# Optimization experiments

Hardware: AMD Instinct MI355X
Metric: run time of the kernel (lower is better)

The kernel has to match this reference:

```python
import jax, jax.numpy as jnp
import numpy as np


def setup_inputs() -> dict:
    key = jax.random.key(0)
    k1, k2, k3 = jax.random.split(key, 3)
    B, L, D, K = 4, 4096, 2048, 4
    x = jax.random.normal(k1, (B, L, D), dtype=jnp.float32)
    # depthwise kernel, channel-last layout (K, 1, D); torch weight is (D,1,K) = w.transpose(2,1,0)
    w = jax.random.normal(k2, (K, 1, D), dtype=jnp.float32) * 0.1
    b = jax.random.normal(k3, (D,), dtype=jnp.float32) * 0.1
    return {"x": x, "w": w, "b": b}


def reference(x, w, b):
    """Depthwise causal conv1d, channel-last.
    x: (B, L, D); w: (K, 1, D); b: (D,). Returns (B, L, D).
    Matches torch: Conv1d(D, D, K, groups=D, padding=K-1)(x.T)[..., :L].T
    which is exactly a causal conv (left pad K-1, trim to L).
    """
    K = w.shape[0]
    D = x.shape[-1]
    y = jax.lax.conv_general_dilated(
        x, w,
        window_strides=(1,),
        padding=[(K - 1, 0)],  # causal: left pad only
        feature_group_count=D,
        dimension_numbers=("NWC", "WIO", "NWC"),
    )
    return y + b
```

## Files before the change

### kernel.cpp

```cpp
#include <hip/hip_runtime.h>
#include <stdint.h>


#define CB 4
#define CL 4096
#define CD 2048
#define STRIP 256
#define HALO 3
#define WROWS 32
#define NSTRIP (CD / STRIP)
#define NSEG (CL / (WROWS * 4))

typedef float nfloat4 __attribute__((ext_vector_type(4)));

__global__ __launch_bounds__(256, 4) void short_conv_kernel(
    const float* __restrict__ x,
    const float* __restrict__ w,
    const float* __restrict__ bias,
    float* __restrict__ y)
{
    const int tid  = threadIdx.x;
    const int lane = tid & 63;
    const int wv   = tid >> 6;

    const int bid   = blockIdx.x;
    const int strip = bid & (NSTRIP - 1);
    const int seg   = (bid >> 3) & (NSEG - 1);
    const int b     = bid >> 8;

    const int r0 = (seg * 4 + wv) * WROWS;
    const int c0 = strip * STRIP;

    const float* xs = x + (size_t)b * CL * CD + c0 + lane * 4;
    float*       ys = y + (size_t)b * CL * CD + c0 + lane * 4;

    const float4 w0 = *(const float4*)(w + 0 * CD + c0 + lane * 4);
    const float4 w1 = *(const float4*)(w + 1 * CD + c0 + lane * 4);
    const float4 w2 = *(const float4*)(w + 2 * CD + c0 + lane * 4);
    const float4 w3 = *(const float4*)(w + 3 * CD + c0 + lane * 4);
    const float4 bv = *(const float4*)(bias + c0 + lane * 4);

    float4 buf[8];
    float4 xm3, xm2, xm1;

    if (r0 > 0) {
        buf[5] = *(const float4*)(xs + (size_t)(r0 - 3) * CD);
        buf[6] = *(const float4*)(xs + (size_t)(r0 - 2) * CD);
        buf[7] = *(const float4*)(xs + (size_t)(r0 - 1) * CD);
    } else {
        buf[5] = buf[6] = buf[7] = make_float4(0.f, 0.f, 0.f, 0.f);
    }
#pragma unroll
    for (int r = 0; r < 5; ++r) {
        buf[r] = *(const float4*)(xs + (size_t)(r0 + r) * CD);
    }
    xm3 = buf[5];
    xm2 = buf[6];
    xm1 = buf[7];

    for (int c = 0; c < 4; ++c) {
#pragma unroll
        for (int t = 0; t < 8; ++t) {
            const int l = r0 + c * 8 + t;

            const int lp = (l + 5 < CL) ? (l + 5) : (CL - 1);
            buf[(t + 5) & 7] = *(const float4*)(xs + (size_t)lp * CD);

            const float4 a0 = buf[t & 7];

            nfloat4 r;
            r.x = fmaf(w0.x, xm3.x, fmaf(w1.x, xm2.x, fmaf(w2.x, xm1.x, fmaf(w3.x, a0.x, bv.x))));
            r.y = fmaf(w0.y, xm3.y, fmaf(w1.y, xm2.y, fmaf(w2.y, xm1.y, fmaf(w3.y, a0.y, bv.y))));
            r.z = fmaf(w0.z, xm3.z, fmaf(w1.z, xm2.z, fmaf(w2.z, xm1.z, fmaf(w3.z, a0.z, bv.z))));
            r.w = fmaf(w0.w, xm3.w, fmaf(w1.w, xm2.w, fmaf(w2.w, xm1.w, fmaf(w3.w, a0.w, bv.w))));

            __builtin_nontemporal_store(r, (nfloat4*)(ys + (size_t)l * CD));

            xm3 = xm2;
            xm2 = xm1;
            xm1 = a0;
        }
    }
}

extern "C" void kernel_launch(void* const* d_in, const int* in_sizes, int n_in,
                              void* d_out, int out_size, void* d_ws, size_t ws_size,
                              hipStream_t stream) {
    const float* x = (const float*)d_in[0];
    const float* w = (const float*)d_in[1];
    const float* b = (const float*)d_in[2];
    float* y = (float*)d_out;

    const int grid = CB * NSTRIP * NSEG;
    short_conv_kernel<<<grid, 256, 0, stream>>>(x, w, b, y);
}
```

Measured before the change: 236.1 us.

## Replace sliding-window strip kernel with grid-stride per-element kernel

Switches from per-wave sliding register windows over 32-row strips to a flat grid-stride loop where each thread computes one float4 output and loads its own three preceding rows. Blocks are swizzled across XCD groups to keep neighbouring rows local in cache. This aims for more uniform parallelism and more memory-level parallelism, but quadruples logical input reads and relies on caches to absorb the halo re-reads.

Result: slower. 244.2 us (+3.4%).

```diff
diff --git a/kernel.cpp b/kernel.cpp
--- a/kernel.cpp
+++ b/kernel.cpp
@@ -5,81 +5,64 @@
 #define CB 4
 #define CL 4096
 #define CD 2048
-#define STRIP 256
-#define HALO 3
-#define WROWS 32
-#define NSTRIP (CD / STRIP)
-#define NSEG (CL / (WROWS * 4))
+#define D4 (CD / 4)
+#define NF4 (CB * CL * CD / 4)
+#define BLK 256
+#define GRID 2048
+#define STEP (BLK * GRID)
+#define STEPS (NF4 / STEP)
 
 typedef float nfloat4 __attribute__((ext_vector_type(4)));
 
-__global__ __launch_bounds__(256, 4) void short_conv_kernel(
+__global__ __launch_bounds__(256) void short_conv_kernel(
     const float* __restrict__ x,
     const float* __restrict__ w,
     const float* __restrict__ bias,
     float* __restrict__ y)
 {
-    const int tid  = threadIdx.x;
-    const int lane = tid & 63;
-    const int wv   = tid >> 6;
+    const int tid = threadIdx.x;
 
-    const int bid   = blockIdx.x;
-    const int strip = bid & (NSTRIP - 1);
-    const int seg   = (bid >> 3) & (NSEG - 1);
-    const int b     = bid >> 8;
+    const int wid = (blockIdx.x & 7) * (GRID / 8) + (blockIdx.x >> 3);
 
-    const int r0 = (seg * 4 + wv) * WROWS;
-    const int c0 = strip * STRIP;
+    const int base4 = wid * BLK + tid;
+    const int d4    = base4 & (D4 - 1);
 
-    const float* xs = x + (size_t)b * CL * CD + c0 + lane * 4;
-    float*       ys = y + (size_t)b * CL * CD + c0 + lane * 4;
+    const float4 w0 = *(const float4*)(w + 0 * CD + d4 * 4);
+    const float4 w1 = *(const float4*)(w + 1 * CD + d4 * 4);
+    const float4 w2 = *(const float4*)(w + 2 * CD + d4 * 4);
+    const float4 w3 = *(const float4*)(w + 3 * CD + d4 * 4);
+    const float4 bv = *(const float4*)(bias + d4 * 4);
 
-    const float4 w0 = *(const float4*)(w + 0 * CD + c0 + lane * 4);
-    const float4 w1 = *(const float4*)(w + 1 * CD + c0 + lane * 4);
-    const float4 w2 = *(const float4*)(w + 2 * CD + c0 + lane * 4);
-    const float4 w3 = *(const float4*)(w + 3 * CD + c0 + lane * 4);
-    const float4 bv = *(const float4*)(bias + c0 + lane * 4);
+    const float4* xf = (const float4*)x;
+    float*        yf = y;
 
-    float4 buf[8];
-    float4 xm3, xm2, xm1;
+#pragma unroll 2
+    for (int s = 0; s < STEPS; ++s) {
+        const int i4 = base4 + s * STEP;
+        const int lb = (i4 >> 9) & (CL - 1);
 
-    if (r0 > 0) {
-        buf[5] = *(const float4*)(xs + (size_t)(r0 - 3) * CD);
-        buf[6] = *(const float4*)(xs + (size_t)(r0 - 2) * CD);
-        buf[7] = *(const float4*)(xs + (size_t)(r0 - 1) * CD);
-    } else {
-        buf[5] = buf[6] = buf[7] = make_float4(0.f, 0.f, 0.f, 0.f);
-    }
-#pragma unroll
-    for (int r = 0; r < 5; ++r) {
-        buf[r] = *(const float4*)(xs + (size_t)(r0 + r) * CD);
-    }
-    xm3 = buf[5];
-    xm2 = buf[6];
-    xm1 = buf[7];
+        const float4* xp = xf + i4;
 
-    for (int c = 0; c < 4; ++c) {
-#pragma unroll
-        for (int t = 0; t < 8; ++t) {
-            const int l = r0 + c * 8 + t;
+        float4 x0 = xp[0];
+        float4 xm1, xm2, xm3;
+        if (lb >= 3) {
+            xm1 = xp[-1 * D4];
+            xm2 = xp[-2 * D4];
+            xm3 = xp[-3 * D4];
+        } else {
+            const float4 z = make_float4(0.f, 0.f, 0.f, 0.f);
+            xm1 = (lb >= 1) ? xp[-1 * D4] : z;
+            xm2 = (lb >= 2) ? xp[-2 * D4] : z;
+            xm3 = z;
+        }
 
-            const int lp = (l + 5 < CL) ? (l + 5) : (CL - 1);
-            buf[(t + 5) & 7] = *(const float4*)(xs + (size_t)lp * CD);
+        nfloat4 r;
+        r.x = fmaf(w0.x, xm3.x, fmaf(w1.x, xm2.x, fmaf(w2.x, xm1.x, fmaf(w3.x, x0.x, bv.x))));
+        r.y = fmaf(w0.y, xm3.y, fmaf(w1.y, xm2.y, fmaf(w2.y, xm1.y, fmaf(w3.y, x0.y, bv.y))));
+        r.z = fmaf(w0.z, xm3.z, fmaf(w1.z, xm2.z, fmaf(w2.z, xm1.z, fmaf(w3.z, x0.z, bv.z))));
+        r.w = fmaf(w0.w, xm3.w, fmaf(w1.w, xm2.w, fmaf(w2.w, xm1.w, fmaf(w3.w, x0.w, bv.w))));
 
-            const float4 a0 = buf[t & 7];
-
-            nfloat4 r;
-            r.x = fmaf(w0.x, xm3.x, fmaf(w1.x, xm2.x, fmaf(w2.x, xm1.x, fmaf(w3.x, a0.x, bv.x))));
-            r.y = fmaf(w0.y, xm3.y, fmaf(w1.y, xm2.y, fmaf(w2.y, xm1.y, fmaf(w3.y, a0.y, bv.y))));
-            r.z = fmaf(w0.z, xm3.z, fmaf(w1.z, xm2.z, fmaf(w2.z, xm1.z, fmaf(w3.z, a0.z, bv.z))));
-            r.w = fmaf(w0.w, xm3.w, fmaf(w1.w, xm2.w, fmaf(w2.w, xm1.w, fmaf(w3.w, a0.w, bv.w))));
-
-            __builtin_nontemporal_store(r, (nfloat4*)(ys + (size_t)l * CD));
-
-            xm3 = xm2;
-            xm2 = xm1;
-            xm1 = a0;
-        }
+        __builtin_nontemporal_store(r, (nfloat4*)(yf + (size_t)i4 * 4));
     }
 }
 
@@ -91,6 +74,5 @@
     const float* b = (const float*)d_in[2];
     float* y = (float*)d_out;
 
-    const int grid = CB * NSTRIP * NSEG;
-    short_conv_kernel<<<grid, 256, 0, stream>>>(x, w, b, y);
+    short_conv_kernel<<<GRID, BLK, 0, stream>>>(x, w, b, y);
 }
```
